# Kernel tuning notes

Hardware: AMD Instinct MI355X
Metric: run time of the kernel (lower is better)

Reference implementation:

```python
import jax, jax.numpy as jnp
import numpy as np
from jax import lax

# Dimensions (match init_kwargs / input_specs)
S, I, NO = 64, 128, 64      # num_states, num_inputs, num_outputs
K, D = 64, 64               # stack_size, stack_dim
B, T_LEN = 64, 256          # batch of sequences, sequence length
PSTR_THRESH = 0.01          # push/pop gating threshold from original code


def setup_inputs() -> dict:
    key = jax.random.key(0)
    k0, k1, k2, k3, k4, k5 = jax.random.split(key, 6)
    return {
        "input_seq": jax.random.randint(k0, (B, T_LEN), 0, I),
        "T": jax.random.normal(k1, (S, I, D, S), jnp.float32) * 0.1,
        "O": jax.random.normal(k2, (S, I, D, NO), jnp.float32) * 0.1,
        "push_gate": jax.random.normal(k3, (S, I, 1), jnp.float32) * 0.1,
        "pop_gate": jax.random.normal(k4, (S, I, 1), jnp.float32) * 0.1,
        "push_value": jax.random.normal(k5, (S, I, D), jnp.float32) * 0.1,
        "init_logits": jnp.zeros((S,), jnp.float32),
    }


def _run_seq(seq, T, O, push_gate, pop_gate, push_value, init_logits):
    """Process one sequence of int symbols; returns [T_LEN, NO] output probs."""
    state0 = jax.nn.softmax(init_logits)                    # (S,)
    content0 = jnp.zeros((K, D), T.dtype)                   # stack buffer
    pointer0 = jnp.zeros((K,), T.dtype).at[0].set(1.0)      # soft stack pointer

    def step(carry, inp):
        state, content, pointer = carry
        stack_top = pointer @ content                       # (D,) soft read

        # Output: mixture over states of softmax(stack_top @ O[s, inp])
        out_logits = jnp.einsum('d,sdo->so', stack_top, O[:, inp])
        out_prob = state @ jax.nn.softmax(out_logits, axis=-1)  # (NO,)

        # Push/pop strengths: scalars; original uses .item() so they are detached
        push_s = lax.stop_gradient(jax.nn.sigmoid(push_gate[:, inp, 0] @ state))
        pop_s = lax.stop_gradient(jax.nn.sigmoid(pop_gate[:, inp, 0] @ state))
        push_v = jnp.tanh(state @ push_value[:, inp, :])    # (D,) keeps grad

        # Pop (only applied if pop_s > threshold, as in original)
        shifted_down = jnp.concatenate([pointer[1:], jnp.zeros((1,), pointer.dtype)])
        ptr_pop = pop_s * shifted_down + (1.0 - pop_s) * pointer
        pointer = jnp.where(pop_s > PSTR_THRESH, ptr_pop, pointer)

        # Push (only applied if push_s > threshold)
        shifted_up = jnp.concatenate([jnp.zeros((1,), pointer.dtype), pointer[:-1]])
        ptr_push = push_s * shifted_up + (1.0 - push_s) * pointer
        w = ptr_push[:, None]                                # (K,1) write weights
        do_push = push_s > PSTR_THRESH
        pointer = jnp.where(do_push, ptr_push, pointer)
        content = jnp.where(do_push, content * (1.0 - w) + push_v[None, :] * w, content)

        # State transition uses PRE-update stack_top (as in original)
        trans_logits = jnp.einsum('d,sdn->sn', stack_top, T[:, inp])
        new_state = state @ jax.nn.softmax(trans_logits, axis=-1)
        return (new_state, content, pointer), out_prob

    _, outs = lax.scan(step, (state0, content0, pointer0), seq)
    return outs


def reference(input_seq, T, O, push_gate, pop_gate, push_value, init_logits):
    run = lambda seq: _run_seq(seq, T, O, push_gate, pop_gate, push_value, init_logits)
    return jax.vmap(run)(input_seq)  # (B, T_LEN, NO)
```

## Files before the change

### kernel.cpp

```cpp
#include <hip/hip_runtime.h>
#include <math.h>

namespace {
constexpr int cS = 64, cI = 128, cNO = 64, cK = 64, cD = 64, cB = 64, cT = 256;
constexpr float cTH = 0.01f;
constexpr int NTASK = cB * cT;
typedef float vf4 __attribute__((ext_vector_type(4)));

__device__ inline void st_agent(float* p, float v) {
    __hip_atomic_store(p, v, __ATOMIC_RELAXED, __HIP_MEMORY_SCOPE_AGENT);
}
__device__ inline float ld_agent(const float* p) {
    return __hip_atomic_load(p, __ATOMIC_RELAXED, __HIP_MEMORY_SCOPE_AGENT);
}

__global__ __launch_bounds__(512, 1)
void p1_kernel(const int* __restrict__ seq,
               const float* __restrict__ Tm,
               const float* __restrict__ pgate,
               const float* __restrict__ qgate,
               const float* __restrict__ pval,
               const float* __restrict__ initl,
               float* __restrict__ stbuf,
               int* __restrict__ cnt,
               float* __restrict__ gpart)
{
    const int b  = blockIdx.x >> 2;
    const int jw = blockIdx.x & 3;
    const int tid = threadIdx.x;
    const int wave = tid >> 6, lane = tid & 63;
    const int dq = lane >> 4, o4 = lane & 15;

    __shared__ float s_state[cS], s_stack[cD], s_pushv[cD], s_pvpart[cD];
    __shared__ float s_ptr[cK], s_w[cK];
    __shared__ float s_content[cK][cD];
    __shared__ float s_redA[8][64], s_redB[8][64], s_npart[8][64];
    __shared__ int   s_seq[cT];
    __shared__ float s_push, s_pop;

    if (wave == 0) {
        float v = initl[lane];
        float m = v;
        #pragma unroll
        for (int sh = 1; sh < 64; sh <<= 1) m = fmaxf(m, __shfl_xor(m, sh));
        float e = expf(v - m);
        float s = e;
        #pragma unroll
        for (int sh = 1; sh < 64; sh <<= 1) s += __shfl_xor(s, sh);
        s_state[lane] = e / s;
    } else if (wave == 1) {
        s_ptr[lane] = (lane == 0) ? 1.0f : 0.0f;
    }
    for (int i = tid; i < cK * cD; i += 512) (&s_content[0][0])[i] = 0.f;
    if (tid < cT) s_seq[tid] = seq[b * cT + tid];
    __syncthreads();

    for (int t = 0; t < cT; ++t) {
        const int inp = s_seq[t];

        {
            float accA = 0.f;
            #pragma unroll
            for (int j = 0; j < 8; ++j) {
                int k = wave * 8 + j;
                accA += s_ptr[k] * s_content[k][lane];
            }
            float accB = 0.f;
            #pragma unroll
            for (int j = 0; j < 2; ++j) {
                int k = jw * 16 + wave * 2 + j;
                accB += s_state[k] * pval[((size_t)k * cI + inp) * cD + lane];
            }
            s_redA[wave][lane] = accA;
            s_redB[wave][lane] = accB;
        }
        __syncthreads();

        float* sb = stbuf + (size_t)(b * cT + t) * 128;
        if (wave == 0) {
            float a = 0.f;
            #pragma unroll
            for (int g = 0; g < 8; ++g) a += s_redA[g][lane];
            s_stack[lane] = a;
            if (jw == 0) sb[lane] = a;
        } else if (wave == 1) {
            float a = 0.f;
            #pragma unroll
            for (int g = 0; g < 8; ++g) a += s_redB[g][lane];
            s_pvpart[lane] = a;
        } else if (wave == 2) {
            float v = pgate[lane * cI + inp] * s_state[lane];
            #pragma unroll
            for (int sh = 1; sh < 64; sh <<= 1) v += __shfl_xor(v, sh);
            if (lane == 0) s_push = 1.0f / (1.0f + expf(-v));
        } else if (wave == 3) {
            float v = qgate[lane * cI + inp] * s_state[lane];
            #pragma unroll
            for (int sh = 1; sh < 64; sh <<= 1) v += __shfl_xor(v, sh);
            if (lane == 0) s_pop = 1.0f / (1.0f + expf(-v));
        } else if (wave == 4) {
            if (jw == 0) sb[64 + lane] = s_state[lane];
        }
        __syncthreads();

        {
            float xs[16];
            #pragma unroll
            for (int i = 0; i < 16; ++i) xs[i] = s_stack[dq * 16 + i];

            const int sA = jw * 16 + wave * 2;
            const int sB = sA + 1;
            const vf4* rpA = reinterpret_cast<const vf4*>(
                Tm + (size_t)(sA * cI + inp) * (cD * cS)) + o4;
            const vf4* rpB = reinterpret_cast<const vf4*>(
                Tm + (size_t)(sB * cI + inp) * (cD * cS)) + o4;
            vf4 va[16], vb[16];
            #pragma unroll
            for (int i = 0; i < 16; ++i) {
                va[i] = rpA[(dq * 16 + i) * 16];
                vb[i] = rpB[(dq * 16 + i) * 16];
            }
            vf4 aA, aB;
            aA.x = 0.f; aA.y = 0.f; aA.z = 0.f; aA.w = 0.f;
            aB.x = 0.f; aB.y = 0.f; aB.z = 0.f; aB.w = 0.f;
            #pragma unroll
            for (int i = 0; i < 16; ++i) {
                float x = xs[i];
                aA.x = fmaf(x, va[i].x, aA.x); aA.y = fmaf(x, va[i].y, aA.y);
                aA.z = fmaf(x, va[i].z, aA.z); aA.w = fmaf(x, va[i].w, aA.w);
                aB.x = fmaf(x, vb[i].x, aB.x); aB.y = fmaf(x, vb[i].y, aB.y);
                aB.z = fmaf(x, vb[i].z, aB.z); aB.w = fmaf(x, vb[i].w, aB.w);
            }
            #pragma unroll
            for (int m = 16; m < 64; m <<= 1) {
                aA.x += __shfl_xor(aA.x, m); aA.y += __shfl_xor(aA.y, m);
                aA.z += __shfl_xor(aA.z, m); aA.w += __shfl_xor(aA.w, m);
                aB.x += __shfl_xor(aB.x, m); aB.y += __shfl_xor(aB.y, m);
                aB.z += __shfl_xor(aB.z, m); aB.w += __shfl_xor(aB.w, m);
            }
            float mA = fmaxf(fmaxf(aA.x, aA.y), fmaxf(aA.z, aA.w));
            float mB = fmaxf(fmaxf(aB.x, aB.y), fmaxf(aB.z, aB.w));
            #pragma unroll
            for (int m = 1; m < 16; m <<= 1) {
                mA = fmaxf(mA, __shfl_xor(mA, m));
                mB = fmaxf(mB, __shfl_xor(mB, m));
            }
            vf4 eA, eB;
            eA.x = expf(aA.x - mA); eA.y = expf(aA.y - mA);
            eA.z = expf(aA.z - mA); eA.w = expf(aA.w - mA);
            eB.x = expf(aB.x - mB); eB.y = expf(aB.y - mB);
            eB.z = expf(aB.z - mB); eB.w = expf(aB.w - mB);
            float smA = eA.x + eA.y + eA.z + eA.w;
            float smB = eB.x + eB.y + eB.z + eB.w;
            #pragma unroll
            for (int m = 1; m < 16; m <<= 1) {
                smA += __shfl_xor(smA, m);
                smB += __shfl_xor(smB, m);
            }
            float cA = s_state[sA] / smA;
            float cB = s_state[sB] / smB;
            vf4 nacc;
            nacc.x = cA * eA.x + cB * eB.x;
            nacc.y = cA * eA.y + cB * eB.y;
            nacc.z = cA * eA.z + cB * eB.z;
            nacc.w = cA * eA.w + cB * eB.w;
            if (dq == 0) {
                s_npart[wave][o4 * 4 + 0] = nacc.x;
                s_npart[wave][o4 * 4 + 1] = nacc.y;
                s_npart[wave][o4 * 4 + 2] = nacc.z;
                s_npart[wave][o4 * 4 + 3] = nacc.w;
            }
        }
        __syncthreads();

        if (wave == 0) {
            float* gq = gpart + ((size_t)(b * 2 + (t & 1)) * 4 + jw) * 128;
            float np = 0.f;
            #pragma unroll
            for (int w = 0; w < 8; ++w) np += s_npart[w][lane];
            st_agent(gq + lane, np);
            st_agent(gq + 64 + lane, s_pvpart[lane]);
            asm volatile("s_waitcnt vmcnt(0)" ::: "memory");
            int* c = cnt + b * cT + t;
            if (lane == 0)
                __hip_atomic_fetch_add(c, 1, __ATOMIC_RELAXED, __HIP_MEMORY_SCOPE_AGENT);
            while (__hip_atomic_load(c, __ATOMIC_RELAXED, __HIP_MEMORY_SCOPE_AGENT) < 4) {}
            const float* gb = gpart + (size_t)(b * 2 + (t & 1)) * 4 * 128;
            float ns = 0.f, pvs = 0.f;
            #pragma unroll
            for (int q = 0; q < 4; ++q) {
                ns  += ld_agent(gb + q * 128 + lane);
                pvs += ld_agent(gb + q * 128 + 64 + lane);
            }
            s_state[lane] = ns;
            s_pushv[lane] = tanhf(pvs);
        } else if (wave == 1) {
            float p  = s_ptr[lane];
            float sd = (lane < cK - 1) ? s_ptr[lane + 1] : 0.f;
            float pop = s_pop;
            float ppo = pop * sd + (1.f - pop) * p;
            float p2  = (pop > cTH) ? ppo : p;
            float su  = __shfl_up(p2, 1);
            if (lane == 0) su = 0.f;
            float push = s_push;
            float ppu = push * su + (1.f - push) * p2;
            s_w[lane] = ppu;
            s_ptr[lane] = (push > cTH) ? ppu : p2;
        }
        __syncthreads();

        if (s_push > cTH) {
            #pragma unroll
            for (int it = 0; it < 8; ++it) {
                int idx = tid + it * 512;
                int k = idx >> 6, d = idx & 63;
                float w = s_w[k];
                s_content[k][d] = s_content[k][d] * (1.f - w) + s_pushv[d] * w;
            }
        }
        __syncthreads();
    }
}

__global__ void k_count(const int* __restrict__ seq, int* __restrict__ counts) {
    int i = blockIdx.x * 256 + threadIdx.x;
    if (i < NTASK) atomicAdd(&counts[seq[i]], 1);
}
__global__ void k_scan(const int* __restrict__ counts, int* __restrict__ offsets,
                       int* __restrict__ cursor) {
    const int lane = threadIdx.x & 63;
    int c0 = counts[lane], c1 = counts[64 + lane];
    int s0 = c0, s1 = c1;
    #pragma unroll
    for (int m = 1; m < 64; m <<= 1) {
        int t0 = __shfl_up(s0, m);
        int t1 = __shfl_up(s1, m);
        if (lane >= m) { s0 += t0; s1 += t1; }
    }
    int tot0 = __shfl(s0, 63);
    int e0 = s0 - c0;
    int e1 = tot0 + s1 - c1;
    offsets[lane] = e0;       cursor[lane] = e0;
    offsets[64 + lane] = e1;  cursor[64 + lane] = e1;
    if (lane == 63) offsets[128] = tot0 + __shfl(s1, 63);
}
__global__ void k_scatter(const int* __restrict__ seq, int* __restrict__ cursor,
                          int* __restrict__ tasks) {
    int i = blockIdx.x * 256 + threadIdx.x;
    if (i < NTASK) {
        int pos = atomicAdd(&cursor[seq[i]], 1);
        tasks[pos] = i;
    }
}

__global__ __launch_bounds__(512, 2)
void p2_kernel(const float* __restrict__ Om,
               const float* __restrict__ stbuf,
               const int* __restrict__ offsets,
               const int* __restrict__ tasks,
               float* __restrict__ out)
{
    const int g = blockIdx.x >> 1, h = blockIdx.x & 1;
    const int tid = threadIdx.x, wave = tid >> 6, lane = tid & 63;
    const int dq = lane >> 4, o4 = lane & 15;

    const int beg = offsets[g], end = offsets[g + 1];
    const int n = end - beg, half = (n + 1) >> 1;
    const int hbeg = beg + h * half;
    const int hend = h ? end : (beg + half);
    const int cnt = hend - hbeg;
    if (cnt <= 0) return;
    const int nsweep = (cnt + 63) >> 6;

    __shared__ vf4 sO[2][1024];

    const vf4* O0 = reinterpret_cast<const vf4*>(Om) + (size_t)g * 1024;
    const size_t rowstride = (size_t)cI * 1024;

    for (int sweep = 0; sweep < nsweep; ++sweep) {
        int   tsk[8];
        bool  val[8];
        float stv[8][16];
        float sstate[8];
        vf4   acc[8];
        #pragma unroll
        for (int u = 0; u < 8; ++u) {
            int idx = hbeg + sweep * 64 + (u >> 2) * 32 + wave * 4 + (u & 3);
            bool v = idx < hend;
            val[u] = v;
            int id = tasks[v ? idx : hbeg];
            id = __builtin_amdgcn_readfirstlane(id);
            tsk[u] = id;
            const float* sp = stbuf + (size_t)id * 128;
            #pragma unroll
            for (int i = 0; i < 16; ++i) stv[u][i] = sp[dq * 16 + i];
            sstate[u] = sp[64 + lane];
            acc[u].x = 0.f; acc[u].y = 0.f; acc[u].z = 0.f; acc[u].w = 0.f;
        }

        vf4 r0 = __builtin_nontemporal_load(O0 + (size_t)tid * 2);
        vf4 r1 = __builtin_nontemporal_load(O0 + (size_t)tid * 2 + 1);

        for (int s = 0; s < cS; ++s) {
            sO[s & 1][tid * 2]     = r0;
            sO[s & 1][tid * 2 + 1] = r1;
            __syncthreads();
            if (s + 1 < cS) {
                const vf4* nr = O0 + (size_t)(s + 1) * rowstride;
                r0 = __builtin_nontemporal_load(nr + (size_t)tid * 2);
                r1 = __builtin_nontemporal_load(nr + (size_t)tid * 2 + 1);
            }
            vf4 part[8];
            #pragma unroll
            for (int u = 0; u < 8; ++u) { part[u].x = 0.f; part[u].y = 0.f; part[u].z = 0.f; part[u].w = 0.f; }
            #pragma unroll
            for (int i = 0; i < 16; ++i) {
                vf4 ovi = sO[s & 1][(dq * 16 + i) * 16 + o4];
                #pragma unroll
                for (int u = 0; u < 8; ++u) {
                    float x = stv[u][i];
                    part[u].x = fmaf(x, ovi.x, part[u].x);
                    part[u].y = fmaf(x, ovi.y, part[u].y);
                    part[u].z = fmaf(x, ovi.z, part[u].z);
                    part[u].w = fmaf(x, ovi.w, part[u].w);
                }
            }
            #pragma unroll
            for (int u = 0; u < 8; ++u) {
                vf4 a = part[u];
                #pragma unroll
                for (int m = 16; m < 64; m <<= 1) {
                    a.x += __shfl_xor(a.x, m); a.y += __shfl_xor(a.y, m);
                    a.z += __shfl_xor(a.z, m); a.w += __shfl_xor(a.w, m);
                }
                float mx = fmaxf(fmaxf(a.x, a.y), fmaxf(a.z, a.w));
                #pragma unroll
                for (int m = 1; m < 16; m <<= 1) mx = fmaxf(mx, __shfl_xor(mx, m));
                vf4 e;
                e.x = expf(a.x - mx); e.y = expf(a.y - mx);
                e.z = expf(a.z - mx); e.w = expf(a.w - mx);
                float sm = e.x + e.y + e.z + e.w;
                #pragma unroll
                for (int m = 1; m < 16; m <<= 1) sm += __shfl_xor(sm, m);
                float coef = __shfl(sstate[u], s) / sm;
                acc[u].x = fmaf(coef, e.x, acc[u].x);
                acc[u].y = fmaf(coef, e.y, acc[u].y);
                acc[u].z = fmaf(coef, e.z, acc[u].z);
                acc[u].w = fmaf(coef, e.w, acc[u].w);
            }
        }
        #pragma unroll
        for (int u = 0; u < 8; ++u) {
            if (val[u] && dq == 0) {
                float* op = out + (size_t)tsk[u] * cNO + o4 * 4;
                op[0] = acc[u].x; op[1] = acc[u].y; op[2] = acc[u].z; op[3] = acc[u].w;
            }
        }
    }
}

__global__ __launch_bounds__(512, 1)
void fpt_mono(const int* __restrict__ seq, const float* __restrict__ Tm,
              const float* __restrict__ Om, const float* __restrict__ pgate,
              const float* __restrict__ qgate, const float* __restrict__ pval,
              const float* __restrict__ initl, float* __restrict__ out)
{
    const int b = blockIdx.x;
    const int tid = threadIdx.x;
    const int wave = tid >> 6, lane = tid & 63;
    const int dq = lane >> 4, o4 = lane & 15;

    __shared__ float s_state[cS], s_nstate[cS], s_stack[cD], s_pushv[cD];
    __shared__ float s_ptr[cK], s_ptr2[cK], s_w[cK];
    __shared__ float s_content[cK][cD];
    __shared__ float s_redA[8][64], s_redB[8][64];
    __shared__ float s_opart[4][cNO], s_npart[4][cS];
    __shared__ float s_push, s_pop;

    if (wave == 0) {
        float v = initl[lane];
        float m = v;
        #pragma unroll
        for (int sh = 1; sh < 64; sh <<= 1) m = fmaxf(m, __shfl_xor(m, sh));
        float e = expf(v - m);
        float s = e;
        #pragma unroll
        for (int sh = 1; sh < 64; sh <<= 1) s += __shfl_xor(s, sh);
        s_state[lane] = e / s;
    } else if (wave == 1) s_ptr[lane] = (lane == 0) ? 1.0f : 0.0f;
    for (int idx = tid; idx < cK * cD; idx += 512) (&s_content[0][0])[idx] = 0.0f;
    __syncthreads();

    for (int t = 0; t < cT; ++t) {
        const int inp = seq[b * cT + t];
        {
            float accA = 0.f, accB = 0.f;
            #pragma unroll
            for (int j = 0; j < 8; ++j) {
                int k = wave * 8 + j;
                accA += s_ptr[k] * s_content[k][lane];
                accB += s_state[k] * pval[(k * cI + inp) * cD + lane];
            }
            s_redA[wave][lane] = accA;
            s_redB[wave][lane] = accB;
        }
        __syncthreads();
        if (wave == 0) {
            float a = 0.f;
            #pragma unroll
            for (int g = 0; g < 8; ++g) a += s_redA[g][lane];
            s_stack[lane] = a;
        } else if (wave == 1) {
            float a = 0.f;
            #pragma unroll
            for (int g = 0; g < 8; ++g) a += s_redB[g][lane];
            s_pushv[lane] = tanhf(a);
        } else if (wave == 2) {
            float v = pgate[lane * cI + inp] * s_state[lane];
            #pragma unroll
            for (int sh = 1; sh < 64; sh <<= 1) v += __shfl_xor(v, sh);
            if (lane == 0) s_push = 1.0f / (1.0f + expf(-v));
        } else if (wave == 3) {
            float v = qgate[lane * cI + inp] * s_state[lane];
            #pragma unroll
            for (int sh = 1; sh < 64; sh <<= 1) v += __shfl_xor(v, sh);
            if (lane == 0) s_pop = 1.0f / (1.0f + expf(-v));
        }
        __syncthreads();
        {
            const bool isO = (wave < 4);
            const int w4 = wave & 3;
            const float* Mbase = isO ? Om : Tm;
            float xs[16];
            #pragma unroll
            for (int i = 0; i < 16; ++i) xs[i] = s_stack[dq * 16 + i];
            float4 oacc = make_float4(0.f, 0.f, 0.f, 0.f);
            for (int r = 0; r < 16; ++r) {
                const int s = w4 * 16 + r;
                const float4* rowp =
                    reinterpret_cast<const float4*>(Mbase + (size_t)(s * cI + inp) * (cD * 64)) + o4;
                float4 acc = make_float4(0.f, 0.f, 0.f, 0.f);
                #pragma unroll
                for (int i = 0; i < 16; ++i) {
                    float4 mv = rowp[(dq * 16 + i) * 16];
                    float xd = xs[i];
                    acc.x = fmaf(xd, mv.x, acc.x); acc.y = fmaf(xd, mv.y, acc.y);
                    acc.z = fmaf(xd, mv.z, acc.z); acc.w = fmaf(xd, mv.w, acc.w);
                }
                #pragma unroll
                for (int m = 16; m < 64; m <<= 1) {
                    acc.x += __shfl_xor(acc.x, m); acc.y += __shfl_xor(acc.y, m);
                    acc.z += __shfl_xor(acc.z, m); acc.w += __shfl_xor(acc.w, m);
                }
                float mx = fmaxf(fmaxf(acc.x, acc.y), fmaxf(acc.z, acc.w));
                #pragma unroll
                for (int m = 1; m < 16; m <<= 1) mx = fmaxf(mx, __shfl_xor(mx, m));
                float4 e;
                e.x = expf(acc.x - mx); e.y = expf(acc.y - mx);
                e.z = expf(acc.z - mx); e.w = expf(acc.w - mx);
                float sm = e.x + e.y + e.z + e.w;
                #pragma unroll
                for (int m = 1; m < 16; m <<= 1) sm += __shfl_xor(sm, m);
                float coef = s_state[s] / sm;
                oacc.x = fmaf(coef, e.x, oacc.x); oacc.y = fmaf(coef, e.y, oacc.y);
                oacc.z = fmaf(coef, e.z, oacc.z); oacc.w = fmaf(coef, e.w, oacc.w);
            }
            if (dq == 0) {
                float* dst = isO ? &s_opart[w4][0] : &s_npart[w4][0];
                dst[o4 * 4 + 0] = oacc.x; dst[o4 * 4 + 1] = oacc.y;
                dst[o4 * 4 + 2] = oacc.z; dst[o4 * 4 + 3] = oacc.w;
            }
        }
        __syncthreads();
        if (wave == 0) {
            float o = s_opart[0][lane] + s_opart[1][lane] + s_opart[2][lane] + s_opart[3][lane];
            out[((size_t)b * cT + t) * cNO + lane] = o;
        } else if (wave == 1) {
            s_nstate[lane] = s_npart[0][lane] + s_npart[1][lane] + s_npart[2][lane] + s_npart[3][lane];
        } else if (wave == 2) {
            float p = s_ptr[lane];
            float sd = (lane < cK - 1) ? s_ptr[lane + 1] : 0.f;
            float pop = s_pop;
            float pp = pop * sd + (1.f - pop) * p;
            s_ptr2[lane] = (pop > cTH) ? pp : p;
        }
        __syncthreads();
        if (wave == 0) {
            float p2 = s_ptr2[lane];
            float su = (lane > 0) ? s_ptr2[lane - 1] : 0.f;
            float push = s_push;
            float pp = push * su + (1.f - push) * p2;
            s_w[lane] = pp;
            s_ptr[lane] = (push > cTH) ? pp : p2;
        } else if (wave == 1) {
            s_state[lane] = s_nstate[lane];
        }
        __syncthreads();
        if (s_push > cTH) {
            for (int idx = tid; idx < cK * cD; idx += 512) {
                int k = idx >> 6, d = idx & 63;
                float w = s_w[k];
                s_content[k][d] = s_content[k][d] * (1.f - w) + s_pushv[d] * w;
            }
        }
        __syncthreads();
    }
}
}

extern "C" void kernel_launch(void* const* d_in, const int* in_sizes, int n_in,
                              void* d_out, int out_size, void* d_ws, size_t ws_size,
                              hipStream_t stream) {
    const int*   seq = (const int*)d_in[0];
    const float* Tm  = (const float*)d_in[1];
    const float* Om  = (const float*)d_in[2];
    const float* pg  = (const float*)d_in[3];
    const float* qg  = (const float*)d_in[4];
    const float* pv  = (const float*)d_in[5];
    const float* il  = (const float*)d_in[6];
    float* o = (float*)d_out;

    const size_t stbuf_bytes  = (size_t)NTASK * 128 * sizeof(float);
    const size_t counts_off   = stbuf_bytes;
    const size_t offsets_off  = counts_off + 128 * sizeof(int);
    const size_t cursor_off   = offsets_off + 132 * sizeof(int);
    const size_t tasks_off    = cursor_off + 128 * sizeof(int);
    const size_t cnt_off      = tasks_off + (size_t)NTASK * sizeof(int);
    const size_t gpart_off    = cnt_off + (size_t)NTASK * sizeof(int);
    const size_t need         = gpart_off + (size_t)cB * 2 * 4 * 128 * sizeof(float);

    if (ws_size < need) {
        hipLaunchKernelGGL(fpt_mono, dim3(cB), dim3(512), 0, stream,
                           seq, Tm, Om, pg, qg, pv, il, o);
        return;
    }

    float* stbuf  = (float*)d_ws;
    int* counts   = (int*)((char*)d_ws + counts_off);
    int* offsets  = (int*)((char*)d_ws + offsets_off);
    int* cursor   = (int*)((char*)d_ws + cursor_off);
    int* tasks    = (int*)((char*)d_ws + tasks_off);
    int* cnt      = (int*)((char*)d_ws + cnt_off);
    float* gpart  = (float*)((char*)d_ws + gpart_off);

    hipMemsetAsync(counts, 0, 128 * sizeof(int), stream);
    hipMemsetAsync(cnt, 0, (size_t)NTASK * sizeof(int), stream);
    hipLaunchKernelGGL(k_count,   dim3(NTASK / 256), dim3(256), 0, stream, seq, counts);
    hipLaunchKernelGGL(k_scan,    dim3(1),           dim3(64),  0, stream, counts, offsets, cursor);
    hipLaunchKernelGGL(k_scatter, dim3(NTASK / 256), dim3(256), 0, stream, seq, cursor, tasks);
    hipLaunchKernelGGL(p1_kernel, dim3(cB * 4), dim3(512), 0, stream,
                       seq, Tm, pg, qg, pv, il, stbuf, cnt, gpart);
    hipLaunchKernelGGL(p2_kernel, dim3(256), dim3(512), 0, stream, Om, stbuf, offsets, tasks, o);
}
```

Measured before the change: 2.969 ms.

## Split each sequence's recurrence across eight 256-thread blocks instead of four

The phase-1 recurrence kernel now divides each sequence's 64 states across 8 cooperating blocks of 256 threads rather than 4 blocks of 512. Each block loads fewer T-matrix rows per step, and 512 blocks can fill more CUs on the MI355X. The cost is a cross-block spin barrier that waits for 8 arrivals each timestep, which means more global atomic traffic and more partials to reduce. It also relies on all 512 blocks being co-resident, since the kernel would deadlock otherwise. Each block also duplicates the stack and content update work, and that work is now spread over fewer threads.

```diff
diff --git a/kernel.cpp b/kernel.cpp
--- a/kernel.cpp
+++ b/kernel.cpp
@@ -5,6 +5,7 @@
 constexpr int cS = 64, cI = 128, cNO = 64, cK = 64, cD = 64, cB = 64, cT = 256;
 constexpr float cTH = 0.01f;
 constexpr int NTASK = cB * cT;
+constexpr int NSPLIT = 8;
 typedef float vf4 __attribute__((ext_vector_type(4)));
 
 __device__ inline void st_agent(float* p, float v) {
@@ -14,7 +15,7 @@
     return __hip_atomic_load(p, __ATOMIC_RELAXED, __HIP_MEMORY_SCOPE_AGENT);
 }
 
-__global__ __launch_bounds__(512, 1)
+__global__ __launch_bounds__(256, 2)
 void p1_kernel(const int* __restrict__ seq,
                const float* __restrict__ Tm,
                const float* __restrict__ pgate,
@@ -25,8 +26,8 @@
                int* __restrict__ cnt,
                float* __restrict__ gpart)
 {
-    const int b  = blockIdx.x >> 2;
-    const int jw = blockIdx.x & 3;
+    const int b  = blockIdx.x >> 3;
+    const int jw = blockIdx.x & 7;
     const int tid = threadIdx.x;
     const int wave = tid >> 6, lane = tid & 63;
     const int dq = lane >> 4, o4 = lane & 15;
@@ -34,7 +35,7 @@
     __shared__ float s_state[cS], s_stack[cD], s_pushv[cD], s_pvpart[cD];
     __shared__ float s_ptr[cK], s_w[cK];
     __shared__ float s_content[cK][cD];
-    __shared__ float s_redA[8][64], s_redB[8][64], s_npart[8][64];
+    __shared__ float s_redA[4][64], s_redB[4][64], s_npart[4][64];
     __shared__ int   s_seq[cT];
     __shared__ float s_push, s_pop;
 
@@ -51,8 +52,8 @@
     } else if (wave == 1) {
         s_ptr[lane] = (lane == 0) ? 1.0f : 0.0f;
     }
-    for (int i = tid; i < cK * cD; i += 512) (&s_content[0][0])[i] = 0.f;
-    if (tid < cT) s_seq[tid] = seq[b * cT + tid];
+    for (int i = tid; i < cK * cD; i += 256) (&s_content[0][0])[i] = 0.f;
+    s_seq[tid] = seq[b * cT + tid];
     __syncthreads();
 
     for (int t = 0; t < cT; ++t) {
@@ -61,14 +62,14 @@
         {
             float accA = 0.f;
             #pragma unroll
-            for (int j = 0; j < 8; ++j) {
-                int k = wave * 8 + j;
+            for (int j = 0; j < 16; ++j) {
+                int k = wave * 16 + j;
                 accA += s_ptr[k] * s_content[k][lane];
             }
             float accB = 0.f;
             #pragma unroll
             for (int j = 0; j < 2; ++j) {
-                int k = jw * 16 + wave * 2 + j;
+                int k = jw * 8 + wave * 2 + j;
                 accB += s_state[k] * pval[((size_t)k * cI + inp) * cD + lane];
             }
             s_redA[wave][lane] = accA;
@@ -78,28 +79,21 @@
 
         float* sb = stbuf + (size_t)(b * cT + t) * 128;
         if (wave == 0) {
-            float a = 0.f;
-            #pragma unroll
-            for (int g = 0; g < 8; ++g) a += s_redA[g][lane];
+            float a = s_redA[0][lane] + s_redA[1][lane] + s_redA[2][lane] + s_redA[3][lane];
             s_stack[lane] = a;
-            if (jw == 0) sb[lane] = a;
+            if (jw == 0) { sb[lane] = a; sb[64 + lane] = s_state[lane]; }
         } else if (wave == 1) {
-            float a = 0.f;
-            #pragma unroll
-            for (int g = 0; g < 8; ++g) a += s_redB[g][lane];
-            s_pvpart[lane] = a;
+            s_pvpart[lane] = s_redB[0][lane] + s_redB[1][lane] + s_redB[2][lane] + s_redB[3][lane];
         } else if (wave == 2) {
             float v = pgate[lane * cI + inp] * s_state[lane];
             #pragma unroll
             for (int sh = 1; sh < 64; sh <<= 1) v += __shfl_xor(v, sh);
             if (lane == 0) s_push = 1.0f / (1.0f + expf(-v));
-        } else if (wave == 3) {
+        } else {
             float v = qgate[lane * cI + inp] * s_state[lane];
             #pragma unroll
             for (int sh = 1; sh < 64; sh <<= 1) v += __shfl_xor(v, sh);
             if (lane == 0) s_pop = 1.0f / (1.0f + expf(-v));
-        } else if (wave == 4) {
-            if (jw == 0) sb[64 + lane] = s_state[lane];
         }
         __syncthreads();
 
@@ -108,7 +102,7 @@
             #pragma unroll
             for (int i = 0; i < 16; ++i) xs[i] = s_stack[dq * 16 + i];
 
-            const int sA = jw * 16 + wave * 2;
+            const int sA = jw * 8 + wave * 2;
             const int sB = sA + 1;
             const vf4* rpA = reinterpret_cast<const vf4*>(
                 Tm + (size_t)(sA * cI + inp) * (cD * cS)) + o4;
@@ -174,21 +168,19 @@
         __syncthreads();
 
         if (wave == 0) {
-            float* gq = gpart + ((size_t)(b * 2 + (t & 1)) * 4 + jw) * 128;
-            float np = 0.f;
-            #pragma unroll
-            for (int w = 0; w < 8; ++w) np += s_npart[w][lane];
+            float* gq = gpart + ((size_t)(b * 2 + (t & 1)) * NSPLIT + jw) * 128;
+            float np = s_npart[0][lane] + s_npart[1][lane] + s_npart[2][lane] + s_npart[3][lane];
             st_agent(gq + lane, np);
             st_agent(gq + 64 + lane, s_pvpart[lane]);
             asm volatile("s_waitcnt vmcnt(0)" ::: "memory");
             int* c = cnt + b * cT + t;
             if (lane == 0)
                 __hip_atomic_fetch_add(c, 1, __ATOMIC_RELAXED, __HIP_MEMORY_SCOPE_AGENT);
-            while (__hip_atomic_load(c, __ATOMIC_RELAXED, __HIP_MEMORY_SCOPE_AGENT) < 4) {}
-            const float* gb = gpart + (size_t)(b * 2 + (t & 1)) * 4 * 128;
+            while (__hip_atomic_load(c, __ATOMIC_RELAXED, __HIP_MEMORY_SCOPE_AGENT) < NSPLIT) {}
+            const float* gb = gpart + (size_t)(b * 2 + (t & 1)) * NSPLIT * 128;
             float ns = 0.f, pvs = 0.f;
             #pragma unroll
-            for (int q = 0; q < 4; ++q) {
+            for (int q = 0; q < NSPLIT; ++q) {
                 ns  += ld_agent(gb + q * 128 + lane);
                 pvs += ld_agent(gb + q * 128 + 64 + lane);
             }
@@ -211,8 +203,8 @@
 
         if (s_push > cTH) {
             #pragma unroll
-            for (int it = 0; it < 8; ++it) {
-                int idx = tid + it * 512;
+            for (int it = 0; it < 16; ++it) {
+                int idx = tid + it * 256;
                 int k = idx >> 6, d = idx & 63;
                 float w = s_w[k];
                 s_content[k][d] = s_content[k][d] * (1.f - w) + s_pushv[d] * w;
@@ -527,7 +519,7 @@
     const size_t tasks_off    = cursor_off + 128 * sizeof(int);
     const size_t cnt_off      = tasks_off + (size_t)NTASK * sizeof(int);
     const size_t gpart_off    = cnt_off + (size_t)NTASK * sizeof(int);
-    const size_t need         = gpart_off + (size_t)cB * 2 * 4 * 128 * sizeof(float);
+    const size_t need         = gpart_off + (size_t)cB * 2 * NSPLIT * 128 * sizeof(float);
 
     if (ws_size < need) {
         hipLaunchKernelGGL(fpt_mono, dim3(cB), dim3(512), 0, stream,
@@ -548,7 +540,7 @@
     hipLaunchKernelGGL(k_count,   dim3(NTASK / 256), dim3(256), 0, stream, seq, counts);
     hipLaunchKernelGGL(k_scan,    dim3(1),           dim3(64),  0, stream, counts, offsets, cursor);
     hipLaunchKernelGGL(k_scatter, dim3(NTASK / 256), dim3(256), 0, stream, seq, cursor, tasks);
-    hipLaunchKernelGGL(p1_kernel, dim3(cB * 4), dim3(512), 0, stream,
+    hipLaunchKernelGGL(p1_kernel, dim3(cB * NSPLIT), dim3(256), 0, stream,
                        seq, Tm, pg, qg, pv, il, stbuf, cnt, gpart);
     hipLaunchKernelGGL(p2_kernel, dim3(256), dim3(512), 0, stream, Om, stbuf, offsets, tasks, o);
 }
```

Measured after the change: 2.690 ms (median of 2 runs). -9.4%, faster.
